# Kernel tuning notes

Hardware: AMD Instinct MI355X
Metric: run time of the kernel (lower is better)

## Reference

```python
import jax, jax.numpy as jnp
import numpy as np

T, B, D, H, L = 1024, 64, 512, 512, 2


def setup_inputs() -> dict:
    key = jax.random.key(0)
    ks = jax.random.split(key, 10)
    s = 1.0 / np.sqrt(D)
    return {
        "x": jax.random.normal(ks[0], (T, B, D), jnp.float32),
        "hidden": jax.random.normal(ks[1], (L, B, H), jnp.float32),
        "fc_w": jax.random.normal(ks[2], (D, D), jnp.float32) * s,
        "fc_b": jax.random.normal(ks[3], (D,), jnp.float32) * s,
        "w0": jax.random.normal(ks[4], (H, D), jnp.float32) * s,
        "b0": jax.random.normal(ks[5], (H,), jnp.float32) * s,
        "u0": jax.random.uniform(ks[6], (H,), jnp.float32, -1.0, 1.0),
        "w1": jax.random.normal(ks[7], (H, H), jnp.float32) * s,
        "b1": jax.random.normal(ks[8], (H,), jnp.float32) * s,
        "u1": jax.random.uniform(ks[9], (H,), jnp.float32, -1.0, 1.0),
    }


def _indrnn_layer(inp, h0, w, b, u):
    # Precompute input projection for all timesteps: [T, B, H]
    pre = jnp.einsum("tbd,hd->tbh", inp, w) + b

    def step(h, p):
        h_new = jax.nn.relu(p + u * h)  # elementwise recurrent weight
        return h_new, h_new

    h_last, outs = jax.lax.scan(step, h0, pre)
    return outs, h_last


def reference(x, hidden, fc_w, fc_b, w0, b0, u0, w1, b1, u1):
    # fc layer before the IndRNN stack
    x = jnp.einsum("tbd,ed->tbe", x, fc_w) + fc_b
    out0, h0 = _indrnn_layer(x, hidden[0], w0, b0, u0)
    out1, h1 = _indrnn_layer(out0, hidden[1], w1, b1, u1)
    hn = jnp.stack([h0, h1], axis=0)  # [L, B, H]
    return out1, hn
```

## Files before the change

kernel.cpp:

```cpp
#include <hip/hip_runtime.h>
#include <hip/hip_bf16.h>
#include <cstdint>
#include <cstddef>

#define T_DIM 1024
#define B_DIM 64
#define D_DIM 512
#define H_DIM 512
#define TBROWS (T_DIM * B_DIM)
#define BH (B_DIM * H_DIM)
#define TBH ((size_t)T_DIM * (size_t)BH)

typedef __bf16 bf16x8 __attribute__((ext_vector_type(8)));
typedef float floatx4 __attribute__((ext_vector_type(4)));

__device__ __forceinline__ void async_load16(const void* g, void* l) {
  __builtin_amdgcn_global_load_lds(
      (const __attribute__((address_space(1))) unsigned int*)g,
      (__attribute__((address_space(3))) unsigned int*)l,
      16, 0, 0);
}

__device__ __forceinline__ void wait_vm(int n) {
  switch (n) {
    case 16: asm volatile("s_waitcnt vmcnt(16)" ::: "memory"); break;
    case 24: asm volatile("s_waitcnt vmcnt(24)" ::: "memory"); break;
    case 32: asm volatile("s_waitcnt vmcnt(32)" ::: "memory"); break;
    case 40: asm volatile("s_waitcnt vmcnt(40)" ::: "memory"); break;
    case 48: asm volatile("s_waitcnt vmcnt(48)" ::: "memory"); break;
    default: asm volatile("s_waitcnt vmcnt(0)" ::: "memory"); break;
  }
}

__global__ __launch_bounds__(256) void prep_kernel(
    const float* __restrict__ w0, const float* __restrict__ fc_w,
    const float* __restrict__ fc_b, const float* __restrict__ b0,
    const float* __restrict__ w1, __bf16* __restrict__ Wc,
    __bf16* __restrict__ w1bf, float* __restrict__ bcomb) {
  const int blk = blockIdx.x;
  const int tid = threadIdx.x;
  if (blk < 128) {
    const int h0 = (blk >> 1) * 8;
    const int d = ((blk & 1) << 8) + tid;
    float a[8];
#pragma unroll
    for (int j = 0; j < 8; j++) a[j] = 0.f;
#pragma unroll 4
    for (int e = 0; e < D_DIM; ++e) {
      const float fv = fc_w[(size_t)e * D_DIM + d];
#pragma unroll
      for (int j = 0; j < 8; j++)
        a[j] = fmaf(w0[(size_t)(h0 + j) * D_DIM + e], fv, a[j]);
    }
#pragma unroll
    for (int j = 0; j < 8; j++)
      Wc[(size_t)(h0 + j) * D_DIM + d] = (__bf16)a[j];
  } else if (blk < 256) {
    const long i = ((long)(blk - 128) * 256 + tid) * 8;
    const float4 a = *(const float4*)(w1 + i);
    const float4 b = *(const float4*)(w1 + i + 4);
    bf16x8 v;
    v[0] = (__bf16)a.x; v[1] = (__bf16)a.y; v[2] = (__bf16)a.z; v[3] = (__bf16)a.w;
    v[4] = (__bf16)b.x; v[5] = (__bf16)b.y; v[6] = (__bf16)b.z; v[7] = (__bf16)b.w;
    *(bf16x8*)(w1bf + i) = v;
  } else {
    const int h = (blk - 256) * 256 + tid;
    float acc = b0[h];
    const float4* w4 = (const float4*)(w0 + (size_t)h * D_DIM);
#pragma unroll 4
    for (int e = 0; e < D_DIM / 4; ++e) {
      const float4 wv = w4[e];
      acc = fmaf(wv.x, fc_b[e * 4 + 0], acc);
      acc = fmaf(wv.y, fc_b[e * 4 + 1], acc);
      acc = fmaf(wv.z, fc_b[e * 4 + 2], acc);
      acc = fmaf(wv.w, fc_b[e * 4 + 3], acc);
    }
    bcomb[h] = acc;
  }
}

#define BM 128
#define BN 128
#define BK 32

__device__ __forceinline__ int xcd_swizzle(int bid, int nwg) {
  return (bid & 7) * (nwg >> 3) + (bid >> 3);
}

__global__ __launch_bounds__(256) void gemm_a32_bt_bias(
    const float* __restrict__ A,
    const __bf16* __restrict__ Bm,
    const float* __restrict__ bias,
    __bf16* __restrict__ C,
    int M, int N, int K) {
  __shared__ float Asf[BM * BK];
  __shared__ __bf16 Bs[BN * BK];

  const int tid = threadIdx.x;
  const int lane = tid & 63;
  const int wave = tid >> 6;
  const int wg = xcd_swizzle((int)blockIdx.x, (int)gridDim.x);
  const int nb = N / BN;
  const int bm = wg / nb;
  const int bn = wg % nb;
  const int m0 = bm * BM, n0 = bn * BN;

  floatx4 zero = {0.f, 0.f, 0.f, 0.f};
  floatx4 acc[4][4];
#pragma unroll
  for (int i = 0; i < 4; i++)
#pragma unroll
    for (int j = 0; j < 4; j++) acc[i][j] = zero;

  const int e0 = (wave * 2 + 0) * 64 + lane;
  const int e1 = (wave * 2 + 1) * 64 + lane;
  const int r0 = e0 >> 2, c0 = (e0 & 3) * 8;
  const int r1 = e1 >> 2, c1 = (e1 & 3) * 8;

  const int tm = (wave >> 1) * 64;
  const int tn = (wave & 1) * 64;
  const int lrow = lane & 15;
  const int lk = (lane >> 4) * 8;

  const int ea = wave * 4;

  for (int k0 = 0; k0 < K; k0 += BK) {
#pragma unroll
    for (int i = 0; i < 4; i++) {
      const int e = (ea + i) * 64 + lane;
      const int r = e >> 3;
      const int sg = (e & 7) ^ (r & 7);
      async_load16(&A[(size_t)(m0 + r) * K + k0 + sg * 4], &Asf[(ea + i) * 256]);
    }
    async_load16(&Bm[(size_t)(n0 + r0) * K + k0 + c0], &Bs[(wave * 2 + 0) * 512]);
    async_load16(&Bm[(size_t)(n0 + r1) * K + k0 + c1], &Bs[(wave * 2 + 1) * 512]);
    __syncthreads();

    bf16x8 af[4], bfr[4];
#pragma unroll
    for (int i = 0; i < 4; i++) {
      const int row = tm + i * 16 + lrow;
      const int k7 = row & 7;
      const int s0 = lk >> 2;
      const float4 fa = *(const float4*)&Asf[row * BK + ((s0 ^ k7) << 2)];
      const float4 fb = *(const float4*)&Asf[row * BK + (((s0 + 1) ^ k7) << 2)];
      bf16x8 v;
      v[0] = (__bf16)fa.x; v[1] = (__bf16)fa.y; v[2] = (__bf16)fa.z; v[3] = (__bf16)fa.w;
      v[4] = (__bf16)fb.x; v[5] = (__bf16)fb.y; v[6] = (__bf16)fb.z; v[7] = (__bf16)fb.w;
      af[i] = v;
      bfr[i] = *(const bf16x8*)&Bs[(tn + i * 16 + lrow) * BK + lk];
    }
#pragma unroll
    for (int i = 0; i < 4; i++)
#pragma unroll
      for (int j = 0; j < 4; j++)
        acc[i][j] = __builtin_amdgcn_mfma_f32_16x16x32_bf16(af[i], bfr[j],
                                                            acc[i][j], 0, 0, 0);
    __syncthreads();
  }

  const int ccol = lane & 15;
  const int crow = (lane >> 4) * 4;
  float bv[4];
#pragma unroll
  for (int j = 0; j < 4; j++) bv[j] = bias[n0 + tn + j * 16 + ccol];
#pragma unroll
  for (int i = 0; i < 4; i++) {
#pragma unroll
    for (int j = 0; j < 4; j++) {
      const size_t base =
          (size_t)(m0 + tm + i * 16 + crow) * N + (n0 + tn + j * 16 + ccol);
#pragma unroll
      for (int r = 0; r < 4; r++)
        C[base + (size_t)r * N] = (__bf16)(acc[i][j][r] + bv[j]);
    }
  }
}

__global__ __launch_bounds__(256) void gemm_bt_bias(
    const __bf16* __restrict__ A,
    const __bf16* __restrict__ Bm,
    const float* __restrict__ bias,
    __bf16* __restrict__ C,
    int M, int N, int K) {
  __shared__ __bf16 As[BM * BK];
  __shared__ __bf16 Bs[BN * BK];

  const int tid = threadIdx.x;
  const int lane = tid & 63;
  const int wave = tid >> 6;
  const int wg = xcd_swizzle((int)blockIdx.x, (int)gridDim.x);
  const int nb = N / BN;
  const int bm = wg / nb;
  const int bn = wg % nb;
  const int m0 = bm * BM, n0 = bn * BN;

  floatx4 zero = {0.f, 0.f, 0.f, 0.f};
  floatx4 acc[4][4];
#pragma unroll
  for (int i = 0; i < 4; i++)
#pragma unroll
    for (int j = 0; j < 4; j++) acc[i][j] = zero;

  const int e0 = (wave * 2 + 0) * 64 + lane;
  const int e1 = (wave * 2 + 1) * 64 + lane;
  const int r0 = e0 >> 2, c0 = (e0 & 3) * 8;
  const int r1 = e1 >> 2, c1 = (e1 & 3) * 8;

  const int tm = (wave >> 1) * 64;
  const int tn = (wave & 1) * 64;
  const int lrow = lane & 15;
  const int lk = (lane >> 4) * 8;

  for (int k0 = 0; k0 < K; k0 += BK) {
    async_load16(&A[(size_t)(m0 + r0) * K + k0 + c0], &As[(wave * 2 + 0) * 512]);
    async_load16(&A[(size_t)(m0 + r1) * K + k0 + c1], &As[(wave * 2 + 1) * 512]);
    async_load16(&Bm[(size_t)(n0 + r0) * K + k0 + c0], &Bs[(wave * 2 + 0) * 512]);
    async_load16(&Bm[(size_t)(n0 + r1) * K + k0 + c1], &Bs[(wave * 2 + 1) * 512]);
    __syncthreads();

    bf16x8 af[4], bfr[4];
#pragma unroll
    for (int i = 0; i < 4; i++) {
      af[i]  = *(const bf16x8*)&As[(tm + i * 16 + lrow) * BK + lk];
      bfr[i] = *(const bf16x8*)&Bs[(tn + i * 16 + lrow) * BK + lk];
    }
#pragma unroll
    for (int i = 0; i < 4; i++)
#pragma unroll
      for (int j = 0; j < 4; j++)
        acc[i][j] = __builtin_amdgcn_mfma_f32_16x16x32_bf16(af[i], bfr[j],
                                                            acc[i][j], 0, 0, 0);
    __syncthreads();
  }

  const int ccol = lane & 15;
  const int crow = (lane >> 4) * 4;
  float bv[4];
#pragma unroll
  for (int j = 0; j < 4; j++) bv[j] = bias[n0 + tn + j * 16 + ccol];
#pragma unroll
  for (int i = 0; i < 4; i++) {
#pragma unroll
    for (int j = 0; j < 4; j++) {
      const size_t base =
          (size_t)(m0 + tm + i * 16 + crow) * N + (n0 + tn + j * 16 + ccol);
#pragma unroll
      for (int r = 0; r < 4; r++)
        C[base + (size_t)r * N] = (__bf16)(acc[i][j][r] + bv[j]);
    }
  }
}

#define TS 64
#define NTILE (T_DIM / TS)

template <bool BF16OUT>
__global__ __launch_bounds__(64, 1) void scan_kernel(
    const __bf16* __restrict__ pre,
    const float* __restrict__ h0,
    const float* __restrict__ u,
    void* __restrict__ outp,
    float* __restrict__ hn) {
  constexpr int OBYTES = BF16OUT ? 2 : 4;
  __shared__ __bf16 tin[3][TS * 64];
  __shared__ char oraw[2][TS * 64 * OBYTES];

  const int lane = threadIdx.x;
  const int c0 = blockIdx.x * 64;
  const int idx = c0 + lane;
  const float uu = u[idx & (H_DIM - 1)];
  float h = h0[idx];

  const int lrow = lane >> 3;
  const int lcg = (lane & 7) * 8;

#pragma unroll
  for (int i = 0; i < 8; i++)
    async_load16(&pre[(size_t)(i * 8 + lrow) * BH + c0 + lcg], &tin[0][i * 512]);
#pragma unroll
  for (int i = 0; i < 8; i++)
    async_load16(&pre[(size_t)(TS + i * 8 + lrow) * BH + c0 + lcg],
                 &tin[1][i * 512]);

  for (int tile = 0; tile < NTILE; ++tile) {
    __builtin_amdgcn_sched_barrier(0);
    if (tile + 2 < NTILE) {
      const int nb = (tile + 2) % 3;
      const size_t nt0 = (size_t)(tile + 2) * TS;
#pragma unroll
      for (int i = 0; i < 8; i++)
        async_load16(&pre[(nt0 + i * 8 + lrow) * BH + c0 + lcg],
                     &tin[nb][i * 512]);
    }
    int wv;
    if (BF16OUT)
      wv = (tile == 0 || tile == NTILE - 1) ? 16
         : (tile == 1 || tile == NTILE - 2) ? 24 : 32;
    else
      wv = (tile == 0) ? 16
         : (tile == 1 || tile == NTILE - 1) ? 32
         : (tile == NTILE - 2) ? 40 : 48;
    wait_vm(wv);
    __builtin_amdgcn_sched_barrier(0);

    const int buf = tile % 3;
    const int t0 = tile * TS;
    char* ob = oraw[tile & 1];
#pragma unroll
    for (int s = 0; s < TS; s++) {
      const float p = (float)tin[buf][s * 64 + lane];
      h = fmaxf(fmaf(uu, h, p), 0.0f);
      if (BF16OUT) ((__bf16*)ob)[s * 64 + lane] = (__bf16)h;
      else         ((float*)ob)[s * 64 + lane] = h;
    }
    if (BF16OUT) {
#pragma unroll
      for (int i = 0; i < 8; i++) {
        const int row = i * 8 + (lane >> 3);
        const bf16x8 v =
            *(const bf16x8*)&((const __bf16*)ob)[row * 64 + (lane & 7) * 8];
        *(bf16x8*)&((__bf16*)outp)[(size_t)(t0 + row) * BH + c0 + (lane & 7) * 8] = v;
      }
    } else {
#pragma unroll
      for (int i = 0; i < 16; i++) {
        const int row = i * 4 + (lane >> 4);
        const float4 v =
            *(const float4*)&((const float*)ob)[row * 64 + (lane & 15) * 4];
        *(float4*)&((float*)outp)[(size_t)(t0 + row) * BH + c0 + (lane & 15) * 4] = v;
      }
    }
  }
  hn[idx] = h;
}

extern "C" void kernel_launch(void* const* d_in, const int* in_sizes, int n_in,
                              void* d_out, int out_size, void* d_ws,
                              size_t ws_size, hipStream_t stream) {
  (void)in_sizes; (void)n_in; (void)out_size; (void)ws_size;
  const float* x      = (const float*)d_in[0];
  const float* hidden = (const float*)d_in[1];
  const float* fc_w   = (const float*)d_in[2];
  const float* fc_b   = (const float*)d_in[3];
  const float* w0     = (const float*)d_in[4];
  const float* b0     = (const float*)d_in[5];
  const float* u0     = (const float*)d_in[6];
  const float* w1     = (const float*)d_in[7];
  const float* b1     = (const float*)d_in[8];
  const float* u1     = (const float*)d_in[9];
  float* out = (float*)d_out;

  char* ws = (char*)d_ws;
  __bf16* pre  = (__bf16*)ws;
  __bf16* out0 = (__bf16*)(ws + TBH * 2);
  char*   tail = ws + 2 * TBH * 2;
  __bf16* Wc    = (__bf16*)tail;
  __bf16* w1bf  = (__bf16*)(tail + 512 * 1024);
  float*  bcomb = (float*)(tail + 1024 * 1024);

  float* hn = out + TBH;

  prep_kernel<<<258, 256, 0, stream>>>(w0, fc_w, fc_b, b0, w1, Wc, w1bf, bcomb);
  gemm_a32_bt_bias<<<(TBROWS / BM) * (H_DIM / BN), 256, 0, stream>>>(
      x, Wc, bcomb, pre, TBROWS, H_DIM, D_DIM);
  scan_kernel<true><<<BH / 64, 64, 0, stream>>>(pre, hidden, u0, (void*)out0, hn);
  gemm_bt_bias<<<(TBROWS / BM) * (H_DIM / BN), 256, 0, stream>>>(
      out0, w1bf, b1, pre, TBROWS, H_DIM, H_DIM);
  scan_kernel<false><<<BH / 64, 64, 0, stream>>>(pre, hidden + BH, u1,
                                                 (void*)out, hn + BH);
}
```

Before: 452.5 us.

## Double-buffer LDS tiles in projection GEMMs and swizzle bf16 tile layout

Both projection GEMM kernels now keep two LDS stages. They issue async global-to-LDS loads for the next K tile before computing on the current one, dropping one barrier per iteration so load latency overlaps MFMA work. The bf16 tiles also get an XOR swizzle on 16-byte chunks, applied consistently on store and read, to cut LDS bank conflicts on the fragment reads. This doubles LDS use per block, which may lower occupancy, and the barrier's implicit wait still bounds how much overlap is possible.

```diff
diff --git a/kernel.cpp b/kernel.cpp
--- a/kernel.cpp
+++ b/kernel.cpp
@@ -93,8 +93,8 @@
     const float* __restrict__ bias,
     __bf16* __restrict__ C,
     int M, int N, int K) {
-  __shared__ float Asf[BM * BK];
-  __shared__ __bf16 Bs[BN * BK];
+  __shared__ float Asf[2][BM * BK];
+  __shared__ __bf16 Bs[2][BN * BK];
 
   const int tid = threadIdx.x;
   const int lane = tid & 63;
@@ -114,41 +114,55 @@
 
   const int e0 = (wave * 2 + 0) * 64 + lane;
   const int e1 = (wave * 2 + 1) * 64 + lane;
-  const int r0 = e0 >> 2, c0 = (e0 & 3) * 8;
-  const int r1 = e1 >> 2, c1 = (e1 & 3) * 8;
+  const int r0 = e0 >> 2, g0 = (e0 & 3) ^ ((r0 >> 1) & 3);
+  const int r1 = e1 >> 2, g1 = (e1 & 3) ^ ((r1 >> 1) & 3);
 
   const int tm = (wave >> 1) * 64;
   const int tn = (wave & 1) * 64;
   const int lrow = lane & 15;
   const int lk = (lane >> 4) * 8;
+  const int sB = lk >> 3;
+  const int s0 = lk >> 2;
 
   const int ea = wave * 4;
 
-  for (int k0 = 0; k0 < K; k0 += BK) {
+  const int KT = K / BK;
+
+  auto stage = [&](int b, int k0) {
 #pragma unroll
     for (int i = 0; i < 4; i++) {
       const int e = (ea + i) * 64 + lane;
       const int r = e >> 3;
-      const int sg = (e & 7) ^ (r & 7);
-      async_load16(&A[(size_t)(m0 + r) * K + k0 + sg * 4], &Asf[(ea + i) * 256]);
-    }
-    async_load16(&Bm[(size_t)(n0 + r0) * K + k0 + c0], &Bs[(wave * 2 + 0) * 512]);
-    async_load16(&Bm[(size_t)(n0 + r1) * K + k0 + c1], &Bs[(wave * 2 + 1) * 512]);
-    __syncthreads();
+      const int g = (e & 7) ^ (r & 7);
+      async_load16(&A[(size_t)(m0 + r) * K + k0 + g * 4],
+                   &Asf[b][(ea + i) * 256]);
+    }
+    async_load16(&Bm[(size_t)(n0 + r0) * K + k0 + g0 * 8],
+                 &Bs[b][(wave * 2 + 0) * 512]);
+    async_load16(&Bm[(size_t)(n0 + r1) * K + k0 + g1 * 8],
+                 &Bs[b][(wave * 2 + 1) * 512]);
+  };
+
+  stage(0, 0);
+  __syncthreads();
+
+  int cur = 0;
+  for (int kt = 0; kt < KT; ++kt) {
+    if (kt + 1 < KT) stage(cur ^ 1, (kt + 1) * BK);
 
     bf16x8 af[4], bfr[4];
 #pragma unroll
     for (int i = 0; i < 4; i++) {
-      const int row = tm + i * 16 + lrow;
-      const int k7 = row & 7;
-      const int s0 = lk >> 2;
-      const float4 fa = *(const float4*)&Asf[row * BK + ((s0 ^ k7) << 2)];
-      const float4 fb = *(const float4*)&Asf[row * BK + (((s0 + 1) ^ k7) << 2)];
+      const int ra = tm + i * 16 + lrow;
+      const int k7 = ra & 7;
+      const float4 fa = *(const float4*)&Asf[cur][ra * 32 + ((s0 ^ k7) << 2)];
+      const float4 fb = *(const float4*)&Asf[cur][ra * 32 + (((s0 + 1) ^ k7) << 2)];
       bf16x8 v;
       v[0] = (__bf16)fa.x; v[1] = (__bf16)fa.y; v[2] = (__bf16)fa.z; v[3] = (__bf16)fa.w;
       v[4] = (__bf16)fb.x; v[5] = (__bf16)fb.y; v[6] = (__bf16)fb.z; v[7] = (__bf16)fb.w;
       af[i] = v;
-      bfr[i] = *(const bf16x8*)&Bs[(tn + i * 16 + lrow) * BK + lk];
+      const int rb = tn + i * 16 + lrow;
+      bfr[i] = *(const bf16x8*)&Bs[cur][rb * 32 + ((sB ^ ((rb >> 1) & 3)) << 3)];
     }
 #pragma unroll
     for (int i = 0; i < 4; i++)
@@ -157,6 +171,7 @@
         acc[i][j] = __builtin_amdgcn_mfma_f32_16x16x32_bf16(af[i], bfr[j],
                                                             acc[i][j], 0, 0, 0);
     __syncthreads();
+    cur ^= 1;
   }
 
   const int ccol = lane & 15;
@@ -183,8 +198,8 @@
     const float* __restrict__ bias,
     __bf16* __restrict__ C,
     int M, int N, int K) {
-  __shared__ __bf16 As[BM * BK];
-  __shared__ __bf16 Bs[BN * BK];
+  __shared__ __bf16 As[2][BM * BK];
+  __shared__ __bf16 Bs[2][BN * BK];
 
   const int tid = threadIdx.x;
   const int lane = tid & 63;
@@ -204,26 +219,42 @@
 
   const int e0 = (wave * 2 + 0) * 64 + lane;
   const int e1 = (wave * 2 + 1) * 64 + lane;
-  const int r0 = e0 >> 2, c0 = (e0 & 3) * 8;
-  const int r1 = e1 >> 2, c1 = (e1 & 3) * 8;
+  const int r0 = e0 >> 2, g0 = (e0 & 3) ^ ((r0 >> 1) & 3);
+  const int r1 = e1 >> 2, g1 = (e1 & 3) ^ ((r1 >> 1) & 3);
 
   const int tm = (wave >> 1) * 64;
   const int tn = (wave & 1) * 64;
   const int lrow = lane & 15;
   const int lk = (lane >> 4) * 8;
-
-  for (int k0 = 0; k0 < K; k0 += BK) {
-    async_load16(&A[(size_t)(m0 + r0) * K + k0 + c0], &As[(wave * 2 + 0) * 512]);
-    async_load16(&A[(size_t)(m0 + r1) * K + k0 + c1], &As[(wave * 2 + 1) * 512]);
-    async_load16(&Bm[(size_t)(n0 + r0) * K + k0 + c0], &Bs[(wave * 2 + 0) * 512]);
-    async_load16(&Bm[(size_t)(n0 + r1) * K + k0 + c1], &Bs[(wave * 2 + 1) * 512]);
-    __syncthreads();
+  const int sB = lk >> 3;
+
+  const int KT = K / BK;
+
+  auto stage = [&](int b, int k0) {
+    async_load16(&A[(size_t)(m0 + r0) * K + k0 + g0 * 8],
+                 &As[b][(wave * 2 + 0) * 512]);
+    async_load16(&A[(size_t)(m0 + r1) * K + k0 + g1 * 8],
+                 &As[b][(wave * 2 + 1) * 512]);
+    async_load16(&Bm[(size_t)(n0 + r0) * K + k0 + g0 * 8],
+                 &Bs[b][(wave * 2 + 0) * 512]);
+    async_load16(&Bm[(size_t)(n0 + r1) * K + k0 + g1 * 8],
+                 &Bs[b][(wave * 2 + 1) * 512]);
+  };
+
+  stage(0, 0);
+  __syncthreads();
+
+  int cur = 0;
+  for (int kt = 0; kt < KT; ++kt) {
+    if (kt + 1 < KT) stage(cur ^ 1, (kt + 1) * BK);
 
     bf16x8 af[4], bfr[4];
 #pragma unroll
     for (int i = 0; i < 4; i++) {
-      af[i]  = *(const bf16x8*)&As[(tm + i * 16 + lrow) * BK + lk];
-      bfr[i] = *(const bf16x8*)&Bs[(tn + i * 16 + lrow) * BK + lk];
+      const int ra = tm + i * 16 + lrow;
+      const int rb = tn + i * 16 + lrow;
+      af[i]  = *(const bf16x8*)&As[cur][ra * 32 + ((sB ^ ((ra >> 1) & 3)) << 3)];
+      bfr[i] = *(const bf16x8*)&Bs[cur][rb * 32 + ((sB ^ ((rb >> 1) & 3)) << 3)];
     }
 #pragma unroll
     for (int i = 0; i < 4; i++)
@@ -232,6 +263,7 @@
         acc[i][j] = __builtin_amdgcn_mfma_f32_16x16x32_bf16(af[i], bfr[j],
                                                             acc[i][j], 0, 0, 0);
     __syncthreads();
+    cur ^= 1;
   }
 
   const int ccol = lane & 15;
```

New measurement: 450.7 us. No clear change (-0.4%).

## Replace GEMMs with 256x256 double-buffered pipelined kernel and pre-convert x to bf16

Applied to the files above, without the earlier changes.

Replaces both projection GEMMs with a single 512-thread kernel using 256x256 tiles, a two-stage double-buffered async global-to-LDS pipeline with partial vmcnt waits, XOR-swizzled LDS layout and raised priority around MFMA issue. The fp32-input GEMM is replaced by a separate conversion pass that writes x as bf16 to workspace, so the main GEMM reads half the bytes per tile. The aim is to overlap loads with MFMA work and raise arithmetic intensity per tile. The cost is an extra full pass over x plus more workspace, and lower occupancy from large LDS use and one block per CU.

```diff
diff --git a/kernel.cpp b/kernel.cpp
--- a/kernel.cpp
+++ b/kernel.cpp
@@ -23,12 +23,28 @@
 
 __device__ __forceinline__ void wait_vm(int n) {
   switch (n) {
+    case 4:  asm volatile("s_waitcnt vmcnt(4)"  ::: "memory"); break;
+    case 8:  asm volatile("s_waitcnt vmcnt(8)"  ::: "memory"); break;
+    case 12: asm volatile("s_waitcnt vmcnt(12)" ::: "memory"); break;
     case 16: asm volatile("s_waitcnt vmcnt(16)" ::: "memory"); break;
     case 24: asm volatile("s_waitcnt vmcnt(24)" ::: "memory"); break;
     case 32: asm volatile("s_waitcnt vmcnt(32)" ::: "memory"); break;
     case 40: asm volatile("s_waitcnt vmcnt(40)" ::: "memory"); break;
     case 48: asm volatile("s_waitcnt vmcnt(48)" ::: "memory"); break;
-    default: asm volatile("s_waitcnt vmcnt(0)" ::: "memory"); break;
+    default: asm volatile("s_waitcnt vmcnt(0)"  ::: "memory"); break;
+  }
+}
+
+__global__ __launch_bounds__(256) void cvt_bf16_kernel(
+    const float* __restrict__ in, __bf16* __restrict__ out, long n) {
+  long i = ((long)blockIdx.x * 256 + threadIdx.x) * 8;
+  if (i + 8 <= n) {
+    const float4 a = *(const float4*)(in + i);
+    const float4 b = *(const float4*)(in + i + 4);
+    bf16x8 v;
+    v[0] = (__bf16)a.x; v[1] = (__bf16)a.y; v[2] = (__bf16)a.z; v[3] = (__bf16)a.w;
+    v[4] = (__bf16)b.x; v[5] = (__bf16)b.y; v[6] = (__bf16)b.z; v[7] = (__bf16)b.w;
+    *(bf16x8*)(out + i) = v;
   }
 }
 
@@ -79,159 +95,88 @@
   }
 }
 
-#define BM 128
-#define BN 128
-#define BK 32
-
 __device__ __forceinline__ int xcd_swizzle(int bid, int nwg) {
   return (bid & 7) * (nwg >> 3) + (bid >> 3);
 }
 
-__global__ __launch_bounds__(256) void gemm_a32_bt_bias(
-    const float* __restrict__ A,
-    const __bf16* __restrict__ Bm,
-    const float* __restrict__ bias,
-    __bf16* __restrict__ C,
-    int M, int N, int K) {
-  __shared__ float Asf[BM * BK];
-  __shared__ __bf16 Bs[BN * BK];
-
-  const int tid = threadIdx.x;
-  const int lane = tid & 63;
-  const int wave = tid >> 6;
-  const int wg = xcd_swizzle((int)blockIdx.x, (int)gridDim.x);
-  const int nb = N / BN;
-  const int bm = wg / nb;
-  const int bn = wg % nb;
-  const int m0 = bm * BM, n0 = bn * BN;
-
-  floatx4 zero = {0.f, 0.f, 0.f, 0.f};
-  floatx4 acc[4][4];
-#pragma unroll
-  for (int i = 0; i < 4; i++)
-#pragma unroll
-    for (int j = 0; j < 4; j++) acc[i][j] = zero;
-
-  const int e0 = (wave * 2 + 0) * 64 + lane;
-  const int e1 = (wave * 2 + 1) * 64 + lane;
-  const int r0 = e0 >> 2, c0 = (e0 & 3) * 8;
-  const int r1 = e1 >> 2, c1 = (e1 & 3) * 8;
-
-  const int tm = (wave >> 1) * 64;
-  const int tn = (wave & 1) * 64;
-  const int lrow = lane & 15;
-  const int lk = (lane >> 4) * 8;
-
-  const int ea = wave * 4;
-
-  for (int k0 = 0; k0 < K; k0 += BK) {
-#pragma unroll
-    for (int i = 0; i < 4; i++) {
-      const int e = (ea + i) * 64 + lane;
-      const int r = e >> 3;
-      const int sg = (e & 7) ^ (r & 7);
-      async_load16(&A[(size_t)(m0 + r) * K + k0 + sg * 4], &Asf[(ea + i) * 256]);
-    }
-    async_load16(&Bm[(size_t)(n0 + r0) * K + k0 + c0], &Bs[(wave * 2 + 0) * 512]);
-    async_load16(&Bm[(size_t)(n0 + r1) * K + k0 + c1], &Bs[(wave * 2 + 1) * 512]);
-    __syncthreads();
-
-    bf16x8 af[4], bfr[4];
-#pragma unroll
-    for (int i = 0; i < 4; i++) {
-      const int row = tm + i * 16 + lrow;
-      const int k7 = row & 7;
-      const int s0 = lk >> 2;
-      const float4 fa = *(const float4*)&Asf[row * BK + ((s0 ^ k7) << 2)];
-      const float4 fb = *(const float4*)&Asf[row * BK + (((s0 + 1) ^ k7) << 2)];
-      bf16x8 v;
-      v[0] = (__bf16)fa.x; v[1] = (__bf16)fa.y; v[2] = (__bf16)fa.z; v[3] = (__bf16)fa.w;
-      v[4] = (__bf16)fb.x; v[5] = (__bf16)fb.y; v[6] = (__bf16)fb.z; v[7] = (__bf16)fb.w;
-      af[i] = v;
-      bfr[i] = *(const bf16x8*)&Bs[(tn + i * 16 + lrow) * BK + lk];
-    }
-#pragma unroll
-    for (int i = 0; i < 4; i++)
-#pragma unroll
-      for (int j = 0; j < 4; j++)
-        acc[i][j] = __builtin_amdgcn_mfma_f32_16x16x32_bf16(af[i], bfr[j],
-                                                            acc[i][j], 0, 0, 0);
-    __syncthreads();
-  }
-
-  const int ccol = lane & 15;
-  const int crow = (lane >> 4) * 4;
-  float bv[4];
-#pragma unroll
-  for (int j = 0; j < 4; j++) bv[j] = bias[n0 + tn + j * 16 + ccol];
-#pragma unroll
-  for (int i = 0; i < 4; i++) {
-#pragma unroll
-    for (int j = 0; j < 4; j++) {
-      const size_t base =
-          (size_t)(m0 + tm + i * 16 + crow) * N + (n0 + tn + j * 16 + ccol);
-#pragma unroll
-      for (int r = 0; r < 4; r++)
-        C[base + (size_t)r * N] = (__bf16)(acc[i][j][r] + bv[j]);
-    }
-  }
-}
-
-__global__ __launch_bounds__(256) void gemm_bt_bias(
+__global__ __launch_bounds__(512, 1) void gemm_bt_bias_8ph(
     const __bf16* __restrict__ A,
     const __bf16* __restrict__ Bm,
     const float* __restrict__ bias,
     __bf16* __restrict__ C,
     int M, int N, int K) {
-  __shared__ __bf16 As[BM * BK];
-  __shared__ __bf16 Bs[BN * BK];
+  __shared__ __bf16 As[2][2][256 * 32];
+  __shared__ __bf16 Bs[2][2][256 * 32];
 
   const int tid = threadIdx.x;
   const int lane = tid & 63;
   const int wave = tid >> 6;
   const int wg = xcd_swizzle((int)blockIdx.x, (int)gridDim.x);
-  const int nb = N / BN;
+  const int nb = N / 256;
   const int bm = wg / nb;
   const int bn = wg % nb;
-  const int m0 = bm * BM, n0 = bn * BN;
+  const int m0 = bm * 256, n0 = bn * 256;
 
   floatx4 zero = {0.f, 0.f, 0.f, 0.f};
-  floatx4 acc[4][4];
-#pragma unroll
-  for (int i = 0; i < 4; i++)
+  floatx4 acc[8][4];
+#pragma unroll
+  for (int i = 0; i < 8; i++)
 #pragma unroll
     for (int j = 0; j < 4; j++) acc[i][j] = zero;
 
-  const int e0 = (wave * 2 + 0) * 64 + lane;
-  const int e1 = (wave * 2 + 1) * 64 + lane;
-  const int r0 = e0 >> 2, c0 = (e0 & 3) * 8;
-  const int r1 = e1 >> 2, c1 = (e1 & 3) * 8;
-
-  const int tm = (wave >> 1) * 64;
-  const int tn = (wave & 1) * 64;
+  const int tm = (wave >> 2) * 128;
+  const int tn = (wave & 3) * 64;
   const int lrow = lane & 15;
-  const int lk = (lane >> 4) * 8;
-
-  for (int k0 = 0; k0 < K; k0 += BK) {
-    async_load16(&A[(size_t)(m0 + r0) * K + k0 + c0], &As[(wave * 2 + 0) * 512]);
-    async_load16(&A[(size_t)(m0 + r1) * K + k0 + c1], &As[(wave * 2 + 1) * 512]);
-    async_load16(&Bm[(size_t)(n0 + r0) * K + k0 + c0], &Bs[(wave * 2 + 0) * 512]);
-    async_load16(&Bm[(size_t)(n0 + r1) * K + k0 + c1], &Bs[(wave * 2 + 1) * 512]);
-    __syncthreads();
-
-    bf16x8 af[4], bfr[4];
-#pragma unroll
-    for (int i = 0; i < 4; i++) {
-      af[i]  = *(const bf16x8*)&As[(tm + i * 16 + lrow) * BK + lk];
-      bfr[i] = *(const bf16x8*)&Bs[(tn + i * 16 + lrow) * BK + lk];
-    }
-#pragma unroll
-    for (int i = 0; i < 4; i++)
+  const int sB = lane >> 4;
+
+  auto S = [&](int t, int c) {
+    const int p = t & 1;
+    const int k0 = t * 64 + c * 32;
+#pragma unroll
+    for (int i = 0; i < 2; i++) {
+      const int u = wave * 2 + i;
+      const int e = u * 64 + lane;
+      const int r = e >> 2;
+      const int g = (e & 3) ^ ((r >> 1) & 3);
+      async_load16(&A[(size_t)(m0 + r) * K + k0 + g * 8], &As[p][c][u * 512]);
+      async_load16(&Bm[(size_t)(n0 + r) * K + k0 + g * 8], &Bs[p][c][u * 512]);
+    }
+  };
+
+  S(0, 0); S(0, 1); S(1, 0); S(1, 1);
+
+  const int F = (K >> 6) << 1;
+  for (int f = 0; f < F; ++f) {
+    const int t = f >> 1, c = f & 1, p = t & 1;
+    if (f >= 1 && f + 3 < F) S((f + 3) >> 1, (f + 3) & 1);
+
+    const int rem = F - 1 - f;
+    wait_vm(rem >= 3 ? 12 : rem * 4);
+    __builtin_amdgcn_s_barrier();
+    __builtin_amdgcn_sched_barrier(0);
+
+    bf16x8 af[8], bfr[4];
+#pragma unroll
+    for (int i = 0; i < 8; i++) {
+      const int ra = tm + i * 16 + lrow;
+      af[i] = *(const bf16x8*)&As[p][c][ra * 32 + ((sB ^ ((ra >> 1) & 3)) << 3)];
+    }
+#pragma unroll
+    for (int j = 0; j < 4; j++) {
+      const int rb = tn + j * 16 + lrow;
+      bfr[j] = *(const bf16x8*)&Bs[p][c][rb * 32 + ((sB ^ ((rb >> 1) & 3)) << 3)];
+    }
+    __builtin_amdgcn_s_setprio(1);
+#pragma unroll
+    for (int i = 0; i < 8; i++)
 #pragma unroll
       for (int j = 0; j < 4; j++)
         acc[i][j] = __builtin_amdgcn_mfma_f32_16x16x32_bf16(af[i], bfr[j],
                                                             acc[i][j], 0, 0, 0);
-    __syncthreads();
+    __builtin_amdgcn_s_setprio(0);
+    __builtin_amdgcn_sched_barrier(0);
+    __builtin_amdgcn_s_barrier();
+    __builtin_amdgcn_sched_barrier(0);
   }
 
   const int ccol = lane & 15;
@@ -240,7 +185,7 @@
 #pragma unroll
   for (int j = 0; j < 4; j++) bv[j] = bias[n0 + tn + j * 16 + ccol];
 #pragma unroll
-  for (int i = 0; i < 4; i++) {
+  for (int i = 0; i < 8; i++) {
 #pragma unroll
     for (int j = 0; j < 4; j++) {
       const size_t base =
@@ -352,9 +297,10 @@
   float* out = (float*)d_out;
 
   char* ws = (char*)d_ws;
-  __bf16* pre  = (__bf16*)ws;
-  __bf16* out0 = (__bf16*)(ws + TBH * 2);
-  char*   tail = ws + 2 * TBH * 2;
+  __bf16* xbf  = (__bf16*)ws;
+  __bf16* pre  = (__bf16*)(ws + TBH * 2);
+  __bf16* out0 = (__bf16*)(ws + 2 * TBH * 2);
+  char*   tail = ws + 3 * TBH * 2;
   __bf16* Wc    = (__bf16*)tail;
   __bf16* w1bf  = (__bf16*)(tail + 512 * 1024);
   float*  bcomb = (float*)(tail + 1024 * 1024);
@@ -362,10 +308,11 @@
   float* hn = out + TBH;
 
   prep_kernel<<<258, 256, 0, stream>>>(w0, fc_w, fc_b, b0, w1, Wc, w1bf, bcomb);
-  gemm_a32_bt_bias<<<(TBROWS / BM) * (H_DIM / BN), 256, 0, stream>>>(
-      x, Wc, bcomb, pre, TBROWS, H_DIM, D_DIM);
+  cvt_bf16_kernel<<<(int)(TBH / (256 * 8)), 256, 0, stream>>>(x, xbf, (long)TBH);
+  gemm_bt_bias_8ph<<<(TBROWS / 256) * (H_DIM / 256), 512, 0, stream>>>(
+      xbf, Wc, bcomb, pre, TBROWS, H_DIM, D_DIM);
   scan_kernel<true><<<BH / 64, 64, 0, stream>>>(pre, hidden, u0, (void*)out0, hn);
-  gemm_bt_bias<<<(TBROWS / BM) * (H_DIM / BN), 256, 0, stream>>>(
+  gemm_bt_bias_8ph<<<(TBROWS / 256) * (H_DIM / 256), 512, 0, stream>>>(
       out0, w1bf, b1, pre, TBROWS, H_DIM, H_DIM);
   scan_kernel<false><<<BH / 64, 64, 0, stream>>>(pre, hidden + BH, u1,
                                                  (void*)out, hn + BH);
```

Result: slower. 468.5 us (+3.5%).
